# Performance work log

Hardware: AMD Instinct MI355X
Metric: run time of the kernel (lower is better)

## Reference

```python
import jax, jax.numpy as jnp
import numpy as np

POOL = 14  # pool_size from __init__


def setup_inputs() -> dict:
    key = jax.random.key(0)
    k1, k2, k3, k4 = jax.random.split(key, 4)
    B, H, W, C, N = 2, 128, 128, 256, 512
    features = jax.random.normal(k1, (B, H, W, C), dtype=jnp.float32)
    # roi layout per original code: [y1, x1, y2, x2]; crop = features[img, x1:x2, y1:y2, :]
    y1 = jax.random.randint(k2, (B, N, 1), 0, H - 16)
    x1 = jax.random.randint(k3, (B, N, 1), 0, W - 16)
    hw = jax.random.randint(k4, (B, N, 2), 8, 16)  # box sizes in [8,16)
    roi = jnp.concatenate([y1, x1, y1 + hw[..., :1], x1 + hw[..., 1:]], axis=-1).astype(jnp.int32)
    return {"features": features, "roi": roi}


def _legacy_resize_axis(start, end, pool):
    """Legacy TF1 bilinear resize (align_corners=False): local src coord = i * (size/pool).
    Returns global low/high integer indices and interpolation fractions, shapes [R, pool]."""
    size = (end - start).astype(jnp.float32)  # [R]
    local = jnp.arange(pool, dtype=jnp.float32)[None, :] * size[:, None] / pool  # [R,P]
    i0 = jnp.floor(local).astype(jnp.int32)
    i1 = jnp.minimum(i0 + 1, (end - start - 1)[:, None])  # clamp inside the crop
    frac = local - i0.astype(jnp.float32)
    return start[:, None] + i0, start[:, None] + i1, frac


def reference(features, roi):
    B, H, W, C = features.shape
    N = roi.shape[1]
    pool = POOL
    roi = roi.reshape(-1, 4)  # [R,4] rows of (y1, x1, y2, x2), R = B*N
    img = jnp.repeat(jnp.arange(B, dtype=jnp.int32), N)  # image index per ROI, [R]
    y1, x1, y2, x2 = roi[:, 0], roi[:, 1], roi[:, 2], roi[:, 3]
    # Original slices rows with x1:x2 and cols with y1:y2; crop+resize == direct
    # bilinear sampling in the full map at global coords start + i*size/pool.
    r0, r1, fr = _legacy_resize_axis(x1, x2, pool)  # rows,   [R,P]
    c0, c1, fc = _legacy_resize_axis(y1, y2, pool)  # cols,   [R,P]

    def gather(r, c):
        # [R,P,P,C] fused gather over all ROIs at once (replaces tf.scan)
        return features[img[:, None, None], r[:, :, None], c[:, None, :], :]

    fr = fr[:, :, None, None]
    fc = fc[:, None, :, None]
    top = gather(r0, c0) * (1.0 - fc) + gather(r0, c1) * fc
    bot = gather(r1, c0) * (1.0 - fc) + gather(r1, c1) * fc
    return top * (1.0 - fr) + bot * fr  # [B*N, pool, pool, C]
```

## Files before the change

### kernel.cpp

```cpp
#include <hip/hip_runtime.h>


typedef float f32x4 __attribute__((ext_vector_type(4)));

#define NROI 1024
#define WAVES_TOTAL (NROI * 14)
#define THREADS 256
#define NBLK (WAVES_TOTAL / 4)

__global__ __launch_bounds__(THREADS) void rpn_pool_kernel(
    const float* __restrict__ feat,
    const int*   __restrict__ roi,
    float*       __restrict__ out)
{
    const int lane = threadIdx.x & 63;
    const int wv   = threadIdx.x >> 6;

    const int d   = blockIdx.x;
    const int blk = (d & 7) * (NBLK / 8) + (d >> 3);
    const int W   = blk * 4 + wv;
    const int q   = W / 14;
    const int j   = W - q * 14;
    const int b   = q >> 9;

    const int4 rr = ((const int4*)roi)[q];
    const int y1 = rr.x, x1 = rr.y, y2 = rr.z, x2 = rr.w;
    const int sR = x2 - x1;
    const int sC = y2 - y1;

    const int pc  = j * sC;
    const int ic0 = pc / 14;
    const float fc  = (float)(pc - ic0 * 14) * (1.0f / 14.0f);
    const float wc1 = 1.0f - fc;
    const int c0 = ic0;
    const int c1 = min(ic0 + 1, sC - 1);

    const size_t SB4 = (size_t)128 * 128 * 64;
    const size_t SR4 = (size_t)128 * 64;
    const f32x4* base = (const f32x4*)feat + (size_t)b * SB4
                        + (size_t)x1 * SR4 + (size_t)y1 * 64 + lane;
    const size_t o0 = (size_t)c0 * 64, o1 = (size_t)c1 * 64;

    int rA = 0, rB = min(1, sR - 1);
    f32x4 a0 = base[o0];
    f32x4 a1 = base[o1];
    f32x4 b0 = base[(size_t)rB * SR4 + o0];
    f32x4 b1 = base[(size_t)rB * SR4 + o1];

    f32x4* outp = (f32x4*)out + ((size_t)q * 196 + j) * 64 + lane;

    for (int i = 0; i < 14; ++i) {
        const int pr = i * sR;
        const float fr = (float)(pr - rA * 14) * (1.0f / 14.0f);

        int nA = rA, nB = rB;
        f32x4 p0, p1;
        bool adv = false;
        if (i < 13) {
            nA = ((i + 1) * sR) / 14;
            nB = min(nA + 1, sR - 1);
            if (nB > rB) {
                p0 = base[(size_t)nB * SR4 + o0];
                p1 = base[(size_t)nB * SR4 + o1];
                adv = true;
            }
        }

        f32x4 o = (a0 * wc1 + a1 * fc) * (1.0f - fr) + (b0 * wc1 + b1 * fc) * fr;

        f32x4* p = outp + (size_t)i * 14 * 64;
        asm volatile("global_store_dwordx4 %0, %1, off sc0 sc1 nt"
                     :: "v"(p), "v"(o) : "memory");

        if (nA > rA) { a0 = b0; a1 = b1; }
        if (adv)     { b0 = p0; b1 = p1; }
        rA = nA; rB = nB;
    }
}

extern "C" void kernel_launch(void* const* d_in, const int* in_sizes, int n_in,
                              void* d_out, int out_size, void* d_ws, size_t ws_size,
                              hipStream_t stream) {
    const float* feat = (const float*)d_in[0];
    const int*   roi  = (const int*)d_in[1];
    float* out = (float*)d_out;

    rpn_pool_kernel<<<NBLK, THREADS, 0, stream>>>(feat, roi, out);
}
```

Measured before the change: 50.32 us.

## Sort ROIs by Morton-coded spatial key to improve feature cache locality

Adds a single-block bitonic sort kernel that orders ROIs by image and a Morton code of their coarse top-left position. The pooling kernel then processes ROIs in this sorted order, so spatially nearby ROIs run close together in time and share feature rows in L2/MALL. This costs an extra kernel launch with a serialized sort and a dependent permutation load before the ROI load. Output positions stay tied to the original ROI index.

Measured after the change: 57.22 us. +13.7%, slower.

```diff
diff --git a/kernel.cpp b/kernel.cpp
--- a/kernel.cpp
+++ b/kernel.cpp
@@ -8,9 +8,40 @@
 #define THREADS 256
 #define NBLK (WAVES_TOTAL / 4)
 
+__device__ __forceinline__ unsigned spread4(unsigned v) {
+    v &= 15u;
+    return (v & 1u) | ((v & 2u) << 1) | ((v & 4u) << 2) | ((v & 8u) << 3);
+}
+
+__global__ __launch_bounds__(1024) void roi_sort_kernel(
+    const int* __restrict__ roi, int* __restrict__ perm)
+{
+    __shared__ unsigned key[NROI];
+    const int t = threadIdx.x;
+    const int4 rr = ((const int4*)roi)[t];
+    const int b = t >> 9;
+    const unsigned m = spread4((unsigned)rr.y >> 3) | (spread4((unsigned)rr.x >> 3) << 1);
+    key[t] = ((((unsigned)b << 8) | m) << 10) | (unsigned)t;
+    __syncthreads();
+    for (int size = 2; size <= NROI; size <<= 1) {
+        for (int stride = size >> 1; stride > 0; stride >>= 1) {
+            const int p = t ^ stride;
+            const unsigned a  = key[t];
+            const unsigned bk = key[p];
+            __syncthreads();
+            const bool asc = ((t & size) == 0);
+            const bool keepmin = ((t < p) == asc);
+            key[t] = keepmin ? min(a, bk) : max(a, bk);
+            __syncthreads();
+        }
+    }
+    perm[t] = (int)(key[t] & 1023u);
+}
+
 __global__ __launch_bounds__(THREADS) void rpn_pool_kernel(
     const float* __restrict__ feat,
     const int*   __restrict__ roi,
+    const int*   __restrict__ perm,
     float*       __restrict__ out)
 {
     const int lane = threadIdx.x & 63;
@@ -19,8 +50,9 @@
     const int d   = blockIdx.x;
     const int blk = (d & 7) * (NBLK / 8) + (d >> 3);
     const int W   = blk * 4 + wv;
-    const int q   = W / 14;
-    const int j   = W - q * 14;
+    const int g   = W / 14;
+    const int j   = W - g * 14;
+    const int q   = perm[g];
     const int b   = q >> 9;
 
     const int4 rr = ((const int4*)roi)[q];
@@ -84,6 +116,8 @@
     const float* feat = (const float*)d_in[0];
     const int*   roi  = (const int*)d_in[1];
     float* out = (float*)d_out;
+    int*   perm = (int*)d_ws;
 
-    rpn_pool_kernel<<<NBLK, THREADS, 0, stream>>>(feat, roi, out);
+    roi_sort_kernel<<<1, 1024, 0, stream>>>(roi, perm);
+    rpn_pool_kernel<<<NBLK, THREADS, 0, stream>>>(feat, roi, perm, out);
 }
```
